# Optimization experiments

Hardware: AMD Instinct MI355X
Metric: run time of the kernel (lower is better)

Reference implementation:

```python
import jax, jax.numpy as jnp
import numpy as np

H, C, L = 4, 64, 3          # heads, out_channels, conv layers
N, E, B = 20000, 320000, 32 # nodes, edges, graphs
HD = 64                     # hidden_dim


def setup_inputs() -> dict:
    key = jax.random.key(0)
    ks = jax.random.split(key, 24)
    x = jax.random.normal(ks[0], (N, 3), jnp.float32)
    src = jax.random.randint(ks[1], (E,), 0, N)
    dst = jax.random.randint(ks[2], (E,), 0, N)
    dst = jnp.where(dst == src, (dst + 1) % N, dst)  # no pre-existing self loops
    edge_index = jnp.stack([src, dst])
    edge_attr = jax.random.normal(ks[3], (E, 4), jnp.float32)
    u = jax.random.normal(ks[4], (B, 10), jnp.float32)
    batch = jnp.sort(jax.random.randint(ks[5], (N,), 0, B))
    p = lambda k, s: jax.random.normal(k, s, jnp.float32) * 0.1
    return {
        'x': x, 'edge_index': edge_index, 'edge_attr': edge_attr, 'u': u, 'batch': batch,
        'node_W': p(ks[6], (3, HD)), 'node_b': p(ks[7], (HD,)),
        'eemb_W': p(ks[8], (4, HD)), 'eemb_b': p(ks[9], (HD,)),
        'lin_W': p(ks[10], (L, HD, H * C)),
        'att_src': p(ks[11], (L, H, C)), 'att_dst': p(ks[12], (L, H, C)),
        'lin_eW': p(ks[13], (L, HD, H * C)), 'att_e': p(ks[14], (L, H, C)),
        'conv_b': p(ks[15], (L, C)),
        'gW': p(ks[16], (10, HD)), 'gb': p(ks[17], (HD,)),
        'f1W': p(ks[18], (2 * HD, HD)), 'f1b': p(ks[19], (HD,)),
        'f2W': p(ks[20], (HD, 2)), 'f2b': p(ks[21], (2,)),
    }


def _gat_layer(x, src, dst, ea, W, a_src, a_dst, We, a_e, b):
    # PyG GATConv(hidden, hidden, edge_dim=hidden, heads=4, concat=False), eval mode
    n = x.shape[0]
    # add self loops; self-loop edge_attr = mean of incoming edge_attr (fill_value='mean')
    deg = jax.ops.segment_sum(jnp.ones_like(dst, dtype=x.dtype), dst, num_segments=n)
    ea_self = jax.ops.segment_sum(ea, dst, num_segments=n) / jnp.maximum(deg, 1.0)[:, None]
    loop = jnp.arange(n)
    src2 = jnp.concatenate([src, loop])
    dst2 = jnp.concatenate([dst, loop])
    ea2 = jnp.concatenate([ea, ea_self], axis=0)
    xp = (x @ W).reshape(n, H, C)                       # [N,H,C]
    a_s = jnp.einsum('nhc,hc->nh', xp, a_src)           # [N,H]
    a_d = jnp.einsum('nhc,hc->nh', xp, a_dst)
    ee = (ea2 @ We).reshape(-1, H, C)                   # [E2,H,C]
    a_ed = jnp.einsum('ehc,hc->eh', ee, a_e)
    alpha = jax.nn.leaky_relu(a_s[src2] + a_d[dst2] + a_ed, 0.2)  # [E2,H]
    # segment softmax over destination nodes (stable)
    m = jax.ops.segment_max(alpha, dst2, num_segments=n)
    ex = jnp.exp(alpha - m[dst2])
    den = jax.ops.segment_sum(ex, dst2, num_segments=n)
    att = ex / den[dst2]
    out = jax.ops.segment_sum(xp[src2] * att[..., None], dst2, num_segments=n)  # [N,H,C]
    return out.mean(axis=1) + b  # concat=False -> mean over heads


def reference(x, edge_index, edge_attr, u, batch, node_W, node_b, eemb_W, eemb_b,
              lin_W, att_src, att_dst, lin_eW, att_e, conv_b, gW, gb, f1W, f1b, f2W, f2b):
    src, dst = edge_index[0], edge_index[1]
    h = jax.nn.relu(x @ node_W + node_b)
    ea = jax.nn.relu(edge_attr @ eemb_W + eemb_b)
    for i in range(L):
        h = jax.nn.relu(_gat_layer(h, src, dst, ea, lin_W[i], att_src[i], att_dst[i],
                                   lin_eW[i], att_e[i], conv_b[i]))
    # global mean pool over graphs
    cnt = jax.ops.segment_sum(jnp.ones((h.shape[0],), h.dtype), batch, num_segments=B)
    pooled = jax.ops.segment_sum(h, batch, num_segments=B) / jnp.maximum(cnt, 1.0)[:, None]
    ug = jax.nn.relu(u @ gW + gb)
    z = jnp.concatenate([pooled, ug], axis=1)
    z = jax.nn.relu(z @ f1W + f1b)
    return z @ f2W + f2b
```

## Files before the change

### kernel.cpp

```cpp
#include <hip/hip_runtime.h>
#include <hip/hip_bf16.h>

#define HD 64

typedef unsigned short u16;

__device__ __forceinline__ float lrelu(float x) { return x > 0.f ? x : 0.2f * x; }
__device__ __forceinline__ int clampi(int v, int maxv) {
    return v < 0 ? 0 : (v >= maxv ? maxv - 1 : v);
}
__device__ __forceinline__ float bf2f(u16 u) {
    return __uint_as_float(((unsigned int)u) << 16);
}
__device__ __forceinline__ u16 f2bf(float f) {
    unsigned int u = __float_as_uint(f);
    unsigned int lsb = (u >> 16) & 1u;
    u += 0x7fffu + lsb;
    return (u16)(u >> 16);
}

__global__ void k_init(const float* __restrict__ x, const float* __restrict__ W,
                       const float* __restrict__ b, float* __restrict__ h,
                       int* deg, int* cursor, int* gcnt, float* pooled, int N, int B) {
    int i = blockIdx.x * blockDim.x + threadIdx.x;
    if (i < N) { deg[i] = 0; cursor[i] = 0; }
    if (i < B) gcnt[i] = 0;
    if (i < B * HD) pooled[i] = 0.f;
    if (i < N * HD) {
        int n = i >> 6, c = i & 63;
        float acc = b[c];
        acc = fmaf(x[n * 3 + 0], W[0 * HD + c], acc);
        acc = fmaf(x[n * 3 + 1], W[1 * HD + c], acc);
        acc = fmaf(x[n * 3 + 2], W[2 * HD + c], acc);
        h[i] = fmaxf(acc, 0.f);
    }
}

__global__ void k_deg(const int* __restrict__ dst, int* __restrict__ deg, int E, int N) {
    int e = blockIdx.x * blockDim.x + threadIdx.x;
    if (e < E) atomicAdd(&deg[clampi(dst[e], N)], 1);
}

__global__ void k_scan1(const int* __restrict__ deg, int* __restrict__ tmp,
                        int* __restrict__ bsum, int N) {
    __shared__ int s[256];
    int tid = threadIdx.x;
    int i = blockIdx.x * 256 + tid;
    int v = (i < N) ? deg[i] : 0;
    s[tid] = v;
    __syncthreads();
    for (int off = 1; off < 256; off <<= 1) {
        int t = (tid >= off) ? s[tid - off] : 0;
        __syncthreads();
        s[tid] += t;
        __syncthreads();
    }
    if (i < N) tmp[i] = s[tid];
    if (tid == 255) bsum[blockIdx.x] = s[255];
}
__global__ void k_scan23(const int* __restrict__ tmp, const int* __restrict__ bsum,
                         int* __restrict__ row_ptr, int N) {
    __shared__ int s_off;
    int t = threadIdx.x;
    if (t < 64) {
        int cnt = blockIdx.x;
        int v = 0;
        for (int base = 0; base < cnt; base += 64)
            if (base + t < cnt) v += bsum[base + t];
        #pragma unroll
        for (int o = 32; o > 0; o >>= 1) v += __shfl_xor(v, o);
        if (t == 0) s_off = v;
    }
    __syncthreads();
    int i = blockIdx.x * 256 + t;
    if (i == 0) row_ptr[0] = 0;
    if (i < N) row_ptr[i + 1] = tmp[i] + s_off;
}

__global__ void k_csr(const int* __restrict__ src, const int* __restrict__ dst,
                      const int* __restrict__ row_ptr, int* __restrict__ cursor,
                      int* __restrict__ csr_src, int* __restrict__ csr_eid, int E, int N) {
    int e = blockIdx.x * blockDim.x + threadIdx.x;
    if (e >= E) return;
    int d = clampi(dst[e], N);
    int pos = row_ptr[d] + atomicAdd(&cursor[d], 1);
    if (pos < E) {
        csr_src[pos] = clampi(src[e], N);
        csr_eid[pos] = e;
    }
}

__global__ __launch_bounds__(256) void k_ee(
    const float* __restrict__ edge_attr, const float* __restrict__ eW,
    const float* __restrict__ eB, const float* __restrict__ lin_eW,
    const float* __restrict__ att_e, const int* __restrict__ csr_eid,
    float* __restrict__ aed, int E) {
    __shared__ float s_ew[256];
    __shared__ float s_eb[64];
    __shared__ float s_wred[768];
    int t = threadIdx.x;
    s_ew[t] = eW[t];
    if (t < 64) s_eb[t] = eB[t];
    for (int idx = t; idx < 768; idx += 256) {
        int l = idx >> 8, hd = idx & 255, hh = hd >> 6, d = hd & 63;
        const float* We = lin_eW + (size_t)l * HD * 256;
        const float* ae = att_e + (size_t)l * 256;
        float acc = 0.f;
        for (int c = 0; c < 64; c++)
            acc = fmaf(We[d * 256 + hh * 64 + c], ae[hh * 64 + c], acc);
        s_wred[idx] = acc;
    }
    __syncthreads();
    int j0 = (blockIdx.x * 256 + t) * 4;
    if (j0 >= E) return;
    float4 a[4];
    int nv = 0;
    #pragma unroll
    for (int q = 0; q < 4; q++) {
        int j = j0 + q;
        if (j < E) {
            a[q] = *(const float4*)(edge_attr + (size_t)csr_eid[j] * 4);
            nv = q + 1;
        } else {
            a[q] = make_float4(0.f, 0.f, 0.f, 0.f);
        }
    }
    float acc[4][12];
    #pragma unroll
    for (int q = 0; q < 4; q++)
        #pragma unroll
        for (int m = 0; m < 12; m++) acc[q][m] = 0.f;
    for (int k = 0; k < HD; k++) {
        float e0 = s_ew[k], e1 = s_ew[64 + k], e2 = s_ew[128 + k], e3 = s_ew[192 + k];
        float eb = s_eb[k];
        float w[12];
        #pragma unroll
        for (int m = 0; m < 12; m++)
            w[m] = s_wred[(m >> 2) * 256 + (m & 3) * 64 + k];
        #pragma unroll
        for (int q = 0; q < 4; q++) {
            float v = fmaf(a[q].x, e0, fmaf(a[q].y, e1,
                      fmaf(a[q].z, e2, fmaf(a[q].w, e3, eb))));
            v = fmaxf(v, 0.f);
            #pragma unroll
            for (int m = 0; m < 12; m++) acc[q][m] = fmaf(v, w[m], acc[q][m]);
        }
    }
    #pragma unroll
    for (int q = 0; q < 4; q++) {
        if (q >= nv) break;
        float* o = aed + (size_t)(j0 + q) * 12;
        #pragma unroll
        for (int m = 0; m < 12; m++) o[m] = acc[q][m];
    }
}

__global__ void k_selfed(const int* __restrict__ row_ptr, float* __restrict__ aed,
                         int E, int N) {
    int n = blockIdx.x * blockDim.x + threadIdx.x;
    if (n >= N) return;
    int r0 = row_ptr[n], r1 = row_ptr[n + 1];
    float acc[12];
    #pragma unroll
    for (int m = 0; m < 12; m++) acc[m] = 0.f;
    for (int j = r0; j < r1; j++) {
        const float* p = aed + (size_t)j * 12;
        #pragma unroll
        for (int m = 0; m < 12; m++) acc[m] += p[m];
    }
    float inv = 1.f / fmaxf((float)(r1 - r0), 1.f);
    float* o = aed + (size_t)(E + n) * 12;
    #pragma unroll
    for (int m = 0; m < 12; m++) o[m] = acc[m] * inv;
}

__global__ __launch_bounds__(256) void k_xp(
    const float* __restrict__ h, const float* __restrict__ W,
    const float* __restrict__ asrc, const float* __restrict__ adst,
    u16* __restrict__ xp, float* __restrict__ a_s, float* __restrict__ a_d, int N) {
    __shared__ float hs[16 * HD];
    int n0 = blockIdx.x * 16;
    int t = threadIdx.x;
    if (n0 + 16 <= N) {
        *(float4*)&hs[t * 4] = *(const float4*)&h[(size_t)n0 * HD + t * 4];
    } else {
        for (int i = t; i < 16 * HD; i += 256) {
            int nn = n0 + (i >> 6);
            hs[i] = (nn < N) ? h[(size_t)nn * HD + (i & 63)] : 0.f;
        }
    }
    __syncthreads();
    int c = t;
    float acc[16];
    #pragma unroll
    for (int k = 0; k < 16; k++) acc[k] = 0.f;
    for (int d = 0; d < HD; d += 4) {
        float w0 = W[(d + 0) * 256 + c];
        float w1 = W[(d + 1) * 256 + c];
        float w2 = W[(d + 2) * 256 + c];
        float w3 = W[(d + 3) * 256 + c];
        #pragma unroll
        for (int k = 0; k < 16; k++) {
            float4 hv = *(const float4*)&hs[k * HD + d];
            acc[k] = fmaf(hv.x, w0, acc[k]);
            acc[k] = fmaf(hv.y, w1, acc[k]);
            acc[k] = fmaf(hv.z, w2, acc[k]);
            acc[k] = fmaf(hv.w, w3, acc[k]);
        }
    }
    float as_ = asrc[c], ad_ = adst[c];
    int hh = c >> 6, cc = c & 63;
    #pragma unroll
    for (int k = 0; k < 16; k++) {
        int nn = n0 + k;
        if (nn >= N) break;
        float ps = acc[k] * as_;
        float pd = acc[k] * ad_;
        #pragma unroll
        for (int o = 32; o > 0; o >>= 1) {
            ps += __shfl_xor(ps, o);
            pd += __shfl_xor(pd, o);
        }
        xp[(size_t)nn * 256 + c] = f2bf(acc[k]);
        if (cc == 0) { a_s[nn * 4 + hh] = ps; a_d[nn * 4 + hh] = pd; }
    }
}

__global__ __launch_bounds__(256) void k_gat(
    const u16* __restrict__ xp, const float* __restrict__ a_s,
    const float* __restrict__ a_d, const float* __restrict__ aed,
    const int* __restrict__ row_ptr, const int* __restrict__ csr_src,
    const float* __restrict__ convb, float* __restrict__ h_out,
    int layer, int N, int E) {
    int wave = threadIdx.x >> 6, lane = threadIdx.x & 63;
    int n = blockIdx.x * 4 + wave;
    if (n >= N) return;
    int g = lane >> 4, p = lane & 15;
    int r0 = row_ptr[n], r1 = row_ptr[n + 1];
    float4 ad4 = *(const float4*)(a_d + (size_t)n * 4);
    float a00 = 0.f, a01 = 0.f, a02 = 0.f, a03 = 0.f;
    float a10 = 0.f, a11 = 0.f, a12 = 0.f, a13 = 0.f;
    float a20 = 0.f, a21 = 0.f, a22 = 0.f, a23 = 0.f;
    float a30 = 0.f, a31 = 0.f, a32 = 0.f, a33 = 0.f;
    float d0 = 0.f, d1 = 0.f, d2 = 0.f, d3 = 0.f;
    if (g == 0) {
        float4 as4 = *(const float4*)(a_s + (size_t)n * 4);
        float4 p4 = *(const float4*)(aed + (size_t)(E + n) * 12 + layer * 4);
        float w0 = __expf(lrelu(as4.x + ad4.x + p4.x));
        float w1 = __expf(lrelu(as4.y + ad4.y + p4.y));
        float w2 = __expf(lrelu(as4.z + ad4.z + p4.z));
        float w3 = __expf(lrelu(as4.w + ad4.w + p4.w));
        const u16* row = xp + (size_t)n * 256 + p * 4;
        ushort4 v0 = *(const ushort4*)(row);
        ushort4 v1 = *(const ushort4*)(row + 64);
        ushort4 v2 = *(const ushort4*)(row + 128);
        ushort4 v3 = *(const ushort4*)(row + 192);
        d0 += w0; d1 += w1; d2 += w2; d3 += w3;
        a00 = fmaf(w0, bf2f(v0.x), a00); a01 = fmaf(w0, bf2f(v0.y), a01);
        a02 = fmaf(w0, bf2f(v0.z), a02); a03 = fmaf(w0, bf2f(v0.w), a03);
        a10 = fmaf(w1, bf2f(v1.x), a10); a11 = fmaf(w1, bf2f(v1.y), a11);
        a12 = fmaf(w1, bf2f(v1.z), a12); a13 = fmaf(w1, bf2f(v1.w), a13);
        a20 = fmaf(w2, bf2f(v2.x), a20); a21 = fmaf(w2, bf2f(v2.y), a21);
        a22 = fmaf(w2, bf2f(v2.z), a22); a23 = fmaf(w2, bf2f(v2.w), a23);
        a30 = fmaf(w3, bf2f(v3.x), a30); a31 = fmaf(w3, bf2f(v3.y), a31);
        a32 = fmaf(w3, bf2f(v3.z), a32); a33 = fmaf(w3, bf2f(v3.w), a33);
    }
    for (int j = r0 + g; j < r1; j += 4) {
        int s = csr_src[j];
        float4 as4 = *(const float4*)(a_s + (size_t)s * 4);
        float4 p4 = *(const float4*)(aed + (size_t)j * 12 + layer * 4);
        float w0 = __expf(lrelu(as4.x + ad4.x + p4.x));
        float w1 = __expf(lrelu(as4.y + ad4.y + p4.y));
        float w2 = __expf(lrelu(as4.z + ad4.z + p4.z));
        float w3 = __expf(lrelu(as4.w + ad4.w + p4.w));
        const u16* row = xp + (size_t)s * 256 + p * 4;
        ushort4 v0 = *(const ushort4*)(row);
        ushort4 v1 = *(const ushort4*)(row + 64);
        ushort4 v2 = *(const ushort4*)(row + 128);
        ushort4 v3 = *(const ushort4*)(row + 192);
        d0 += w0; d1 += w1; d2 += w2; d3 += w3;
        a00 = fmaf(w0, bf2f(v0.x), a00); a01 = fmaf(w0, bf2f(v0.y), a01);
        a02 = fmaf(w0, bf2f(v0.z), a02); a03 = fmaf(w0, bf2f(v0.w), a03);
        a10 = fmaf(w1, bf2f(v1.x), a10); a11 = fmaf(w1, bf2f(v1.y), a11);
        a12 = fmaf(w1, bf2f(v1.z), a12); a13 = fmaf(w1, bf2f(v1.w), a13);
        a20 = fmaf(w2, bf2f(v2.x), a20); a21 = fmaf(w2, bf2f(v2.y), a21);
        a22 = fmaf(w2, bf2f(v2.z), a22); a23 = fmaf(w2, bf2f(v2.w), a23);
        a30 = fmaf(w3, bf2f(v3.x), a30); a31 = fmaf(w3, bf2f(v3.y), a31);
        a32 = fmaf(w3, bf2f(v3.z), a32); a33 = fmaf(w3, bf2f(v3.w), a33);
    }
    d0 += __shfl_xor(d0, 16); d0 += __shfl_xor(d0, 32);
    d1 += __shfl_xor(d1, 16); d1 += __shfl_xor(d1, 32);
    d2 += __shfl_xor(d2, 16); d2 += __shfl_xor(d2, 32);
    d3 += __shfl_xor(d3, 16); d3 += __shfl_xor(d3, 32);
    float i0 = 1.f / d0, i1 = 1.f / d1, i2 = 1.f / d2, i3 = 1.f / d3;
    float m0 = a00 * i0 + a10 * i1 + a20 * i2 + a30 * i3;
    float m1 = a01 * i0 + a11 * i1 + a21 * i2 + a31 * i3;
    float m2 = a02 * i0 + a12 * i1 + a22 * i2 + a32 * i3;
    float m3 = a03 * i0 + a13 * i1 + a23 * i2 + a33 * i3;
    m0 += __shfl_xor(m0, 16); m0 += __shfl_xor(m0, 32);
    m1 += __shfl_xor(m1, 16); m1 += __shfl_xor(m1, 32);
    m2 += __shfl_xor(m2, 16); m2 += __shfl_xor(m2, 32);
    m3 += __shfl_xor(m3, 16); m3 += __shfl_xor(m3, 32);
    if (lane < 16) {
        int c = p * 4;
        h_out[(size_t)n * HD + c + 0] = fmaxf(0.25f * m0 + convb[c + 0], 0.f);
        h_out[(size_t)n * HD + c + 1] = fmaxf(0.25f * m1 + convb[c + 1], 0.f);
        h_out[(size_t)n * HD + c + 2] = fmaxf(0.25f * m2 + convb[c + 2], 0.f);
        h_out[(size_t)n * HD + c + 3] = fmaxf(0.25f * m3 + convb[c + 3], 0.f);
    }
}

#define PCHUNK 4
__global__ void k_pool(const float* __restrict__ h, const int* __restrict__ batch,
                       float* __restrict__ pooled, int* __restrict__ gcnt, int N, int B) {
    int b = blockIdx.x / PCHUNK, q = blockIdx.x % PCHUNK;
    __shared__ int sb[2];
    __shared__ float sred[256];
    int t = threadIdx.x;
    if (t == 0 || t == 64) {
        int target = b + (t ? 1 : 0);
        int lo = 0, hi = N;
        while (lo < hi) {
            int m = (lo + hi) >> 1;
            if (batch[m] < target) lo = m + 1; else hi = m;
        }
        sb[t ? 1 : 0] = lo;
    }
    __syncthreads();
    int start = sb[0], end = sb[1];
    int len = end - start;
    if (q == 0 && t == 0) gcnt[b] = len;
    int c0 = start + (int)(((long long)len * q) / PCHUNK);
    int c1 = start + (int)(((long long)len * (q + 1)) / PCHUNK);
    int c = t & 63, r = t >> 6;
    float acc = 0.f;
    for (int nidx = c0 + r; nidx < c1; nidx += 4)
        acc += h[(size_t)nidx * HD + c];
    sred[t] = acc;
    __syncthreads();
    if (t < 64) {
        float v = sred[t] + sred[64 + t] + sred[128 + t] + sred[192 + t];
        atomicAdd(&pooled[b * HD + c], v);
    }
}

__global__ void k_mlp(const float* __restrict__ u, const float* __restrict__ gW,
                      const float* __restrict__ gb, const float* __restrict__ pooled,
                      const int* __restrict__ gcnt, const float* __restrict__ f1W,
                      const float* __restrict__ f1b, const float* __restrict__ f2W,
                      const float* __restrict__ f2b, float* __restrict__ out, int B) {
    __shared__ float z[2 * HD];
    __shared__ float z1s[HD];
    int b = blockIdx.x, t = threadIdx.x;
    float acc = gb[t];
    for (int k = 0; k < 10; k++) acc = fmaf(u[b * 10 + k], gW[k * HD + t], acc);
    z[HD + t] = fmaxf(acc, 0.f);
    float invc = 1.f / fmaxf((float)gcnt[b], 1.f);
    z[t] = pooled[b * HD + t] * invc;
    __syncthreads();
    float a1 = f1b[t];
    for (int k = 0; k < 2 * HD; k++) a1 = fmaf(z[k], f1W[k * HD + t], a1);
    z1s[t] = fmaxf(a1, 0.f);
    __syncthreads();
    if (t < 2) {
        float o = f2b[t];
        for (int k = 0; k < HD; k++) o = fmaf(z1s[k], f2W[k * 2 + t], o);
        out[b * 2 + t] = o;
    }
}

extern "C" void kernel_launch(void* const* d_in, const int* in_sizes, int n_in,
                              void* d_out, int out_size, void* d_ws, size_t ws_size,
                              hipStream_t stream) {
    const float* x         = (const float*)d_in[0];
    const int*   ei        = (const int*)d_in[1];
    const float* edge_attr = (const float*)d_in[2];
    const float* u         = (const float*)d_in[3];
    const int*   batch     = (const int*)d_in[4];
    const float* node_W    = (const float*)d_in[5];
    const float* node_b    = (const float*)d_in[6];
    const float* eemb_W    = (const float*)d_in[7];
    const float* eemb_b    = (const float*)d_in[8];
    const float* lin_W     = (const float*)d_in[9];
    const float* att_src   = (const float*)d_in[10];
    const float* att_dst   = (const float*)d_in[11];
    const float* lin_eW    = (const float*)d_in[12];
    const float* att_e     = (const float*)d_in[13];
    const float* conv_b    = (const float*)d_in[14];
    const float* gW        = (const float*)d_in[15];
    const float* gb        = (const float*)d_in[16];
    const float* f1W       = (const float*)d_in[17];
    const float* f1b       = (const float*)d_in[18];
    const float* f2W       = (const float*)d_in[19];
    const float* f2b       = (const float*)d_in[20];

    const int N = in_sizes[0] / 3;
    const int E = in_sizes[2] / 4;
    const int B = in_sizes[3] / 10;
    const int* src = ei;
    const int* dst = ei + E;
    const int NB = (N + 255) / 256;

    float* wsf = (float*)d_ws;
    float* h       = wsf;              wsf += (size_t)N * HD;
    float* a_s     = wsf;              wsf += (size_t)N * 4;
    float* a_d     = wsf;              wsf += (size_t)N * 4;
    float* aed     = wsf;              wsf += (size_t)(E + N) * 12;
    float* pooled  = wsf;              wsf += (size_t)B * HD;
    u16* xp = (u16*)wsf;               wsf += (size_t)N * 128;
    int* wsi = (int*)wsf;
    int* deg     = wsi;                wsi += N;
    int* row_ptr = wsi;                wsi += N + 1;
    int* cursor  = wsi;                wsi += N;
    int* tmp     = wsi;                wsi += N;
    int* bsum    = wsi;                wsi += NB + 1;
    int* csr_src = wsi;                wsi += E;
    int* csr_eid = wsi;                wsi += E;
    int* gcnt    = wsi;                wsi += B;

    k_init<<<(N * HD + 255) / 256, 256, 0, stream>>>(x, node_W, node_b, h,
                                                     deg, cursor, gcnt, pooled, N, B);
    k_deg<<<(E + 255) / 256, 256, 0, stream>>>(dst, deg, E, N);
    k_scan1<<<NB, 256, 0, stream>>>(deg, tmp, bsum, N);
    k_scan23<<<NB, 256, 0, stream>>>(tmp, bsum, row_ptr, N);
    k_csr<<<(E + 255) / 256, 256, 0, stream>>>(src, dst, row_ptr, cursor,
                                               csr_src, csr_eid, E, N);
    k_ee<<<(E + 1023) / 1024, 256, 0, stream>>>(edge_attr, eemb_W, eemb_b, lin_eW, att_e,
                                                csr_eid, aed, E);
    k_selfed<<<NB, 256, 0, stream>>>(row_ptr, aed, E, N);
    for (int i = 0; i < 3; i++) {
        k_xp<<<(N + 15) / 16, 256, 0, stream>>>(h, lin_W + (size_t)i * HD * 256,
                                                att_src + (size_t)i * 256,
                                                att_dst + (size_t)i * 256,
                                                xp, a_s, a_d, N);
        k_gat<<<(N + 3) / 4, 256, 0, stream>>>(xp, a_s, a_d, aed, row_ptr, csr_src,
                                               conv_b + (size_t)i * HD, h, i, N, E);
    }
    k_pool<<<B * PCHUNK, 256, 0, stream>>>(h, batch, pooled, gcnt, N, B);
    k_mlp<<<B, 64, 0, stream>>>(u, gW, gb, pooled, gcnt, f1W, f1b, f2W, f2b,
                                (float*)d_out, B);
}
```

Measured before the change: 382.8 us.

## Split edge attention per layer, pack CSR pairs, retile xp, fuse pool+MLP

The per-edge attention term is stored as three layer-major planes of float4 instead of one interleaved 12-float record, so each GAT layer reads a contiguous 16-byte stream. The CSR source and edge-id arrays are packed into one int2 array, and the GAT loop prefetches the next entry. k_xp now handles 32 nodes per block and reads h directly from global memory instead of staging it in shared memory. Pooling and the MLP are fused into a single kernel with one block per graph, which removes the atomics and the extra launch but lowers parallelism in the pooling step.

```diff
diff --git a/kernel.cpp b/kernel.cpp
--- a/kernel.cpp
+++ b/kernel.cpp
@@ -21,11 +21,9 @@
 
 __global__ void k_init(const float* __restrict__ x, const float* __restrict__ W,
                        const float* __restrict__ b, float* __restrict__ h,
-                       int* deg, int* cursor, int* gcnt, float* pooled, int N, int B) {
+                       int* deg, int* cursor, int N) {
     int i = blockIdx.x * blockDim.x + threadIdx.x;
     if (i < N) { deg[i] = 0; cursor[i] = 0; }
-    if (i < B) gcnt[i] = 0;
-    if (i < B * HD) pooled[i] = 0.f;
     if (i < N * HD) {
         int n = i >> 6, c = i & 63;
         float acc = b[c];
@@ -79,25 +77,23 @@
 
 __global__ void k_csr(const int* __restrict__ src, const int* __restrict__ dst,
                       const int* __restrict__ row_ptr, int* __restrict__ cursor,
-                      int* __restrict__ csr_src, int* __restrict__ csr_eid, int E, int N) {
+                      int2* __restrict__ csr_se, int E, int N) {
     int e = blockIdx.x * blockDim.x + threadIdx.x;
     if (e >= E) return;
     int d = clampi(dst[e], N);
     int pos = row_ptr[d] + atomicAdd(&cursor[d], 1);
-    if (pos < E) {
-        csr_src[pos] = clampi(src[e], N);
-        csr_eid[pos] = e;
-    }
+    if (pos < E) csr_se[pos] = make_int2(clampi(src[e], N), e);
 }
 
 __global__ __launch_bounds__(256) void k_ee(
     const float* __restrict__ edge_attr, const float* __restrict__ eW,
     const float* __restrict__ eB, const float* __restrict__ lin_eW,
-    const float* __restrict__ att_e, const int* __restrict__ csr_eid,
-    float* __restrict__ aed, int E) {
+    const float* __restrict__ att_e, const int2* __restrict__ csr_se,
+    float* __restrict__ aed, int E, int N) {
     __shared__ float s_ew[256];
     __shared__ float s_eb[64];
     __shared__ float s_wred[768];
+    size_t P4 = (size_t)(E + N) * 4;
     int t = threadIdx.x;
     s_ew[t] = eW[t];
     if (t < 64) s_eb[t] = eB[t];
@@ -119,7 +115,7 @@
     for (int q = 0; q < 4; q++) {
         int j = j0 + q;
         if (j < E) {
-            a[q] = *(const float4*)(edge_attr + (size_t)csr_eid[j] * 4);
+            a[q] = *(const float4*)(edge_attr + (size_t)csr_se[j].y * 4);
             nv = q + 1;
         } else {
             a[q] = make_float4(0.f, 0.f, 0.f, 0.f);
@@ -149,9 +145,12 @@
     #pragma unroll
     for (int q = 0; q < 4; q++) {
         if (q >= nv) break;
-        float* o = aed + (size_t)(j0 + q) * 12;
-        #pragma unroll
-        for (int m = 0; m < 12; m++) o[m] = acc[q][m];
+        #pragma unroll
+        for (int l = 0; l < 3; l++) {
+            *(float4*)(aed + l * P4 + (size_t)(j0 + q) * 4) =
+                make_float4(acc[q][l * 4 + 0], acc[q][l * 4 + 1],
+                            acc[q][l * 4 + 2], acc[q][l * 4 + 3]);
+        }
     }
 }
 
@@ -159,49 +158,49 @@
                          int E, int N) {
     int n = blockIdx.x * blockDim.x + threadIdx.x;
     if (n >= N) return;
+    size_t P4 = (size_t)(E + N) * 4;
     int r0 = row_ptr[n], r1 = row_ptr[n + 1];
     float acc[12];
     #pragma unroll
     for (int m = 0; m < 12; m++) acc[m] = 0.f;
     for (int j = r0; j < r1; j++) {
-        const float* p = aed + (size_t)j * 12;
-        #pragma unroll
-        for (int m = 0; m < 12; m++) acc[m] += p[m];
+        #pragma unroll
+        for (int l = 0; l < 3; l++) {
+            float4 v = *(const float4*)(aed + l * P4 + (size_t)j * 4);
+            acc[l * 4 + 0] += v.x; acc[l * 4 + 1] += v.y;
+            acc[l * 4 + 2] += v.z; acc[l * 4 + 3] += v.w;
+        }
     }
     float inv = 1.f / fmaxf((float)(r1 - r0), 1.f);
-    float* o = aed + (size_t)(E + n) * 12;
-    #pragma unroll
-    for (int m = 0; m < 12; m++) o[m] = acc[m] * inv;
-}
-
+    #pragma unroll
+    for (int l = 0; l < 3; l++) {
+        *(float4*)(aed + l * P4 + (size_t)(E + n) * 4) =
+            make_float4(acc[l * 4 + 0] * inv, acc[l * 4 + 1] * inv,
+                        acc[l * 4 + 2] * inv, acc[l * 4 + 3] * inv);
+    }
+}
+
+#define NPB 32
 __global__ __launch_bounds__(256) void k_xp(
     const float* __restrict__ h, const float* __restrict__ W,
     const float* __restrict__ asrc, const float* __restrict__ adst,
     u16* __restrict__ xp, float* __restrict__ a_s, float* __restrict__ a_d, int N) {
-    __shared__ float hs[16 * HD];
-    int n0 = blockIdx.x * 16;
-    int t = threadIdx.x;
-    if (n0 + 16 <= N) {
-        *(float4*)&hs[t * 4] = *(const float4*)&h[(size_t)n0 * HD + t * 4];
-    } else {
-        for (int i = t; i < 16 * HD; i += 256) {
-            int nn = n0 + (i >> 6);
-            hs[i] = (nn < N) ? h[(size_t)nn * HD + (i & 63)] : 0.f;
-        }
-    }
-    __syncthreads();
-    int c = t;
-    float acc[16];
-    #pragma unroll
-    for (int k = 0; k < 16; k++) acc[k] = 0.f;
+    int n0 = blockIdx.x * NPB;
+    int c = threadIdx.x;
+    int nlim = N - n0;
+    const float* hp = h + (size_t)n0 * HD;
+    float acc[NPB];
+    #pragma unroll
+    for (int k = 0; k < NPB; k++) acc[k] = 0.f;
     for (int d = 0; d < HD; d += 4) {
         float w0 = W[(d + 0) * 256 + c];
         float w1 = W[(d + 1) * 256 + c];
         float w2 = W[(d + 2) * 256 + c];
         float w3 = W[(d + 3) * 256 + c];
         #pragma unroll
-        for (int k = 0; k < 16; k++) {
-            float4 hv = *(const float4*)&hs[k * HD + d];
+        for (int k = 0; k < NPB; k++) {
+            int kk = (k < nlim) ? k : 0;
+            float4 hv = *(const float4*)(hp + kk * HD + d);
             acc[k] = fmaf(hv.x, w0, acc[k]);
             acc[k] = fmaf(hv.y, w1, acc[k]);
             acc[k] = fmaf(hv.z, w2, acc[k]);
@@ -211,7 +210,7 @@
     float as_ = asrc[c], ad_ = adst[c];
     int hh = c >> 6, cc = c & 63;
     #pragma unroll
-    for (int k = 0; k < 16; k++) {
+    for (int k = 0; k < NPB; k++) {
         int nn = n0 + k;
         if (nn >= N) break;
         float ps = acc[k] * as_;
@@ -228,10 +227,9 @@
 
 __global__ __launch_bounds__(256) void k_gat(
     const u16* __restrict__ xp, const float* __restrict__ a_s,
-    const float* __restrict__ a_d, const float* __restrict__ aed,
-    const int* __restrict__ row_ptr, const int* __restrict__ csr_src,
-    const float* __restrict__ convb, float* __restrict__ h_out,
-    int layer, int N, int E) {
+    const float* __restrict__ a_d, const float* __restrict__ aedl,
+    const int* __restrict__ row_ptr, const int2* __restrict__ csr_se,
+    const float* __restrict__ convb, float* __restrict__ h_out, int N, int E) {
     int wave = threadIdx.x >> 6, lane = threadIdx.x & 63;
     int n = blockIdx.x * 4 + wave;
     if (n >= N) return;
@@ -245,7 +243,7 @@
     float d0 = 0.f, d1 = 0.f, d2 = 0.f, d3 = 0.f;
     if (g == 0) {
         float4 as4 = *(const float4*)(a_s + (size_t)n * 4);
-        float4 p4 = *(const float4*)(aed + (size_t)(E + n) * 12 + layer * 4);
+        float4 p4 = *(const float4*)(aedl + (size_t)(E + n) * 4);
         float w0 = __expf(lrelu(as4.x + ad4.x + p4.x));
         float w1 = __expf(lrelu(as4.y + ad4.y + p4.y));
         float w2 = __expf(lrelu(as4.z + ad4.z + p4.z));
@@ -265,10 +263,14 @@
         a30 = fmaf(w3, bf2f(v3.x), a30); a31 = fmaf(w3, bf2f(v3.y), a31);
         a32 = fmaf(w3, bf2f(v3.z), a32); a33 = fmaf(w3, bf2f(v3.w), a33);
     }
-    for (int j = r0 + g; j < r1; j += 4) {
-        int s = csr_src[j];
+    int j = r0 + g;
+    int2 se = (j < r1) ? csr_se[j] : make_int2(0, 0);
+    for (; j < r1; j += 4) {
+        int jn = j + 4;
+        int2 se_n = (jn < r1) ? csr_se[jn] : make_int2(0, 0);
+        int s = se.x;
         float4 as4 = *(const float4*)(a_s + (size_t)s * 4);
-        float4 p4 = *(const float4*)(aed + (size_t)j * 12 + layer * 4);
+        float4 p4 = *(const float4*)(aedl + (size_t)j * 4);
         float w0 = __expf(lrelu(as4.x + ad4.x + p4.x));
         float w1 = __expf(lrelu(as4.y + ad4.y + p4.y));
         float w2 = __expf(lrelu(as4.z + ad4.z + p4.z));
@@ -287,6 +289,7 @@
         a22 = fmaf(w2, bf2f(v2.z), a22); a23 = fmaf(w2, bf2f(v2.w), a23);
         a30 = fmaf(w3, bf2f(v3.x), a30); a31 = fmaf(w3, bf2f(v3.y), a31);
         a32 = fmaf(w3, bf2f(v3.z), a32); a33 = fmaf(w3, bf2f(v3.w), a33);
+        se = se_n;
     }
     d0 += __shfl_xor(d0, 16); d0 += __shfl_xor(d0, 32);
     d1 += __shfl_xor(d1, 16); d1 += __shfl_xor(d1, 32);
@@ -310,12 +313,17 @@
     }
 }
 
-#define PCHUNK 4
-__global__ void k_pool(const float* __restrict__ h, const int* __restrict__ batch,
-                       float* __restrict__ pooled, int* __restrict__ gcnt, int N, int B) {
-    int b = blockIdx.x / PCHUNK, q = blockIdx.x % PCHUNK;
+__global__ __launch_bounds__(256) void k_poolmlp(
+    const float* __restrict__ h, const int* __restrict__ batch,
+    const float* __restrict__ u, const float* __restrict__ gW,
+    const float* __restrict__ gb, const float* __restrict__ f1W,
+    const float* __restrict__ f1b, const float* __restrict__ f2W,
+    const float* __restrict__ f2b, float* __restrict__ out, int N, int B) {
+    int b = blockIdx.x;
     __shared__ int sb[2];
     __shared__ float sred[256];
+    __shared__ float z[2 * HD];
+    __shared__ float z1s[HD];
     int t = threadIdx.x;
     if (t == 0 || t == 64) {
         int target = b + (t ? 1 : 0);
@@ -327,40 +335,26 @@
         sb[t ? 1 : 0] = lo;
     }
     __syncthreads();
-    int start = sb[0], end = sb[1];
-    int len = end - start;
-    if (q == 0 && t == 0) gcnt[b] = len;
-    int c0 = start + (int)(((long long)len * q) / PCHUNK);
-    int c1 = start + (int)(((long long)len * (q + 1)) / PCHUNK);
+    int start = sb[0], end = sb[1], len = end - start;
     int c = t & 63, r = t >> 6;
     float acc = 0.f;
-    for (int nidx = c0 + r; nidx < c1; nidx += 4)
+    for (int nidx = start + r; nidx < end; nidx += 4)
         acc += h[(size_t)nidx * HD + c];
     sred[t] = acc;
     __syncthreads();
     if (t < 64) {
-        float v = sred[t] + sred[64 + t] + sred[128 + t] + sred[192 + t];
-        atomicAdd(&pooled[b * HD + c], v);
-    }
-}
-
-__global__ void k_mlp(const float* __restrict__ u, const float* __restrict__ gW,
-                      const float* __restrict__ gb, const float* __restrict__ pooled,
-                      const int* __restrict__ gcnt, const float* __restrict__ f1W,
-                      const float* __restrict__ f1b, const float* __restrict__ f2W,
-                      const float* __restrict__ f2b, float* __restrict__ out, int B) {
-    __shared__ float z[2 * HD];
-    __shared__ float z1s[HD];
-    int b = blockIdx.x, t = threadIdx.x;
-    float acc = gb[t];
-    for (int k = 0; k < 10; k++) acc = fmaf(u[b * 10 + k], gW[k * HD + t], acc);
-    z[HD + t] = fmaxf(acc, 0.f);
-    float invc = 1.f / fmaxf((float)gcnt[b], 1.f);
-    z[t] = pooled[b * HD + t] * invc;
-    __syncthreads();
-    float a1 = f1b[t];
-    for (int k = 0; k < 2 * HD; k++) a1 = fmaf(z[k], f1W[k * HD + t], a1);
-    z1s[t] = fmaxf(a1, 0.f);
+        float inv = 1.f / fmaxf((float)len, 1.f);
+        z[t] = (sred[t] + sred[64 + t] + sred[128 + t] + sred[192 + t]) * inv;
+        float a = gb[t];
+        for (int k = 0; k < 10; k++) a = fmaf(u[b * 10 + k], gW[k * HD + t], a);
+        z[HD + t] = fmaxf(a, 0.f);
+    }
+    __syncthreads();
+    if (t < 64) {
+        float a1 = f1b[t];
+        for (int k = 0; k < 2 * HD; k++) a1 = fmaf(z[k], f1W[k * HD + t], a1);
+        z1s[t] = fmaxf(a1, 0.f);
+    }
     __syncthreads();
     if (t < 2) {
         float o = f2b[t];
@@ -400,43 +394,41 @@
     const int* src = ei;
     const int* dst = ei + E;
     const int NB = (N + 255) / 256;
+    const size_t P4 = (size_t)(E + N) * 4;
 
     float* wsf = (float*)d_ws;
     float* h       = wsf;              wsf += (size_t)N * HD;
     float* a_s     = wsf;              wsf += (size_t)N * 4;
     float* a_d     = wsf;              wsf += (size_t)N * 4;
-    float* aed     = wsf;              wsf += (size_t)(E + N) * 12;
-    float* pooled  = wsf;              wsf += (size_t)B * HD;
+    float* aed     = wsf;              wsf += 3 * P4;
     u16* xp = (u16*)wsf;               wsf += (size_t)N * 128;
     int* wsi = (int*)wsf;
+    int2* csr_se = (int2*)wsi;         wsi += 2 * (size_t)E;
     int* deg     = wsi;                wsi += N;
     int* row_ptr = wsi;                wsi += N + 1;
     int* cursor  = wsi;                wsi += N;
     int* tmp     = wsi;                wsi += N;
     int* bsum    = wsi;                wsi += NB + 1;
-    int* csr_src = wsi;                wsi += E;
-    int* csr_eid = wsi;                wsi += E;
-    int* gcnt    = wsi;                wsi += B;
 
     k_init<<<(N * HD + 255) / 256, 256, 0, stream>>>(x, node_W, node_b, h,
-                                                     deg, cursor, gcnt, pooled, N, B);
+                                                     deg, cursor, N);
     k_deg<<<(E + 255) / 256, 256, 0, stream>>>(dst, deg, E, N);
     k_scan1<<<NB, 256, 0, stream>>>(deg, tmp, bsum, N);
     k_scan23<<<NB, 256, 0, stream>>>(tmp, bsum, row_ptr, N);
     k_csr<<<(E + 255) / 256, 256, 0, stream>>>(src, dst, row_ptr, cursor,
-                                               csr_src, csr_eid, E, N);
+                                               csr_se, E, N);
     k_ee<<<(E + 1023) / 1024, 256, 0, stream>>>(edge_attr, eemb_W, eemb_b, lin_eW, att_e,
-                                                csr_eid, aed, E);
+                                                csr_se, aed, E, N);
     k_selfed<<<NB, 256, 0, stream>>>(row_ptr, aed, E, N);
     for (int i = 0; i < 3; i++) {
-        k_xp<<<(N + 15) / 16, 256, 0, stream>>>(h, lin_W + (size_t)i * HD * 256,
-                                                att_src + (size_t)i * 256,
-                                                att_dst + (size_t)i * 256,
-                                                xp, a_s, a_d, N);
-        k_gat<<<(N + 3) / 4, 256, 0, stream>>>(xp, a_s, a_d, aed, row_ptr, csr_src,
-                                               conv_b + (size_t)i * HD, h, i, N, E);
-    }
-    k_pool<<<B * PCHUNK, 256, 0, stream>>>(h, batch, pooled, gcnt, N, B);
-    k_mlp<<<B, 64, 0, stream>>>(u, gW, gb, pooled, gcnt, f1W, f1b, f2W, f2b,
-                                (float*)d_out, B);
-}
+        k_xp<<<(N + NPB - 1) / NPB, 256, 0, stream>>>(h, lin_W + (size_t)i * HD * 256,
+                                                      att_src + (size_t)i * 256,
+                                                      att_dst + (size_t)i * 256,
+                                                      xp, a_s, a_d, N);
+        k_gat<<<(N + 3) / 4, 256, 0, stream>>>(xp, a_s, a_d, aed + (size_t)i * P4,
+                                               row_ptr, csr_se,
+                                               conv_b + (size_t)i * HD, h, N, E);
+    }
+    k_poolmlp<<<B, 256, 0, stream>>>(h, batch, u, gW, gb, f1W, f1b, f2W, f2b,
+                                     (float*)d_out, N, B);
+}
```

Result: slower. 492.1 us (+28.6%).
